# Kernel optimization log

Hardware: AMD Instinct MI355X
Metric: run time of the kernel (lower is better)

## Reference

```python
import jax, jax.numpy as jnp
import numpy as np

N_DATA = 500_000
FEAT_DIM = 512
NUM_CLASS = 10_000
BATCH = 8192
MOMENTUM = 0.9


def setup_inputs() -> dict:
    key = jax.random.key(0)
    k1, k2, k3, k4 = jax.random.split(key, 4)
    stdv = 1.0 / np.sqrt(FEAT_DIM / 3)
    # lat_memory initialized as randn * 2*stdv - stdv (matches torch init)
    lat_memory = jax.random.normal(k1, (N_DATA, FEAT_DIM), dtype=jnp.float32) * (2 * stdv) - stdv
    batch_samples = jax.random.normal(k2, (BATCH, FEAT_DIM), dtype=jnp.float32)
    targets = jax.random.randint(k3, (BATCH,), 0, NUM_CLASS)
    # unique dataset indices (each training sample has one memory slot)
    idx = jax.random.permutation(k4, N_DATA)[:BATCH]
    class_sums = jnp.zeros((NUM_CLASS, FEAT_DIM), dtype=jnp.float32)
    return {
        "batch_samples": batch_samples,
        "lat_memory": lat_memory,
        "class_sums": class_sums,
        "targets": targets,
        "idx": idx,
    }


def reference(batch_samples, lat_memory, class_sums, targets, idx):
    # gather rows, momentum blend, L2 normalize
    blended = lat_memory[idx] * (1.0 - MOMENTUM) + batch_samples * MOMENTUM  # [B, D]
    norm = jnp.sqrt(jnp.sum(blended * blended, axis=1, keepdims=True))
    updated = blended / norm  # [B, D]
    # scatter normalized rows back into the memory bank
    new_lat_memory = lat_memory.at[idx].set(updated)
    # per-class segment sum (replaces python loop over unique labels)
    new_class_sums = class_sums + jax.ops.segment_sum(updated, targets, num_segments=NUM_CLASS)
    return new_lat_memory, new_class_sums
```

## Files before the change

kernel.cpp:

```cpp
#include <hip/hip_runtime.h>

#define N_DATA    500000
#define FEAT_DIM  512
#define NUM_CLASS 10000
#define BATCH     8192
#define MOMENTUM  0.9f

__global__ __launch_bounds__(256) void copy_f4_kernel(const float4* __restrict__ src,
                                                      float4* __restrict__ dst,
                                                      long long n4) {
    long long i = (long long)blockIdx.x * blockDim.x + threadIdx.x;
    long long stride = (long long)gridDim.x * blockDim.x;
    for (; i < n4; i += stride) {
        dst[i] = src[i];
    }
}

__global__ __launch_bounds__(128) void update_kernel(const float4* __restrict__ batch,
                                                     const float4* __restrict__ lat,
                                                     const int*    __restrict__ targets,
                                                     const int*    __restrict__ idx,
                                                     float4*       __restrict__ out_lat,
                                                     float*        __restrict__ out_cls)
{
    const int row = blockIdx.x;
    const int t   = threadIdx.x;

    const int src_row = idx[row];
    const int cls     = targets[row];

    const float4 b = batch[(long long)row * 128 + t];
    const float4 m = lat[(long long)src_row * 128 + t];

    float4 v;
    v.x = m.x * (1.0f - MOMENTUM) + b.x * MOMENTUM;
    v.y = m.y * (1.0f - MOMENTUM) + b.y * MOMENTUM;
    v.z = m.z * (1.0f - MOMENTUM) + b.z * MOMENTUM;
    v.w = m.w * (1.0f - MOMENTUM) + b.w * MOMENTUM;

    float ss = v.x * v.x + v.y * v.y + v.z * v.z + v.w * v.w;

    #pragma unroll
    for (int off = 32; off > 0; off >>= 1) {
        ss += __shfl_down(ss, off, 64);
    }

    __shared__ float partial[2];
    if ((t & 63) == 0) partial[t >> 6] = ss;
    __syncthreads();
    const float total = partial[0] + partial[1];
    const float inv = 1.0f / sqrtf(total);

    v.x *= inv; v.y *= inv; v.z *= inv; v.w *= inv;

    out_lat[(long long)src_row * 128 + t] = v;

    float* cp = out_cls + (long long)cls * FEAT_DIM + t * 4;
    atomicAdd(cp + 0, v.x);
    atomicAdd(cp + 1, v.y);
    atomicAdd(cp + 2, v.z);
    atomicAdd(cp + 3, v.w);
}

extern "C" void kernel_launch(void* const* d_in, const int* in_sizes, int n_in,
                              void* d_out, int out_size, void* d_ws, size_t ws_size,
                              hipStream_t stream) {
    const float* batch    = (const float*)d_in[0];
    const float* lat      = (const float*)d_in[1];
    const float* cls_sums = (const float*)d_in[2];
    const int*   targets  = (const int*)d_in[3];
    const int*   idx      = (const int*)d_in[4];

    float* out_lat = (float*)d_out;
    float* out_cls = out_lat + (long long)N_DATA * FEAT_DIM;

    {
        long long n4 = (long long)N_DATA * FEAT_DIM / 4;
        int blocks = 8192;
        copy_f4_kernel<<<blocks, 256, 0, stream>>>((const float4*)lat, (float4*)out_lat, n4);
    }

    {
        long long n4 = (long long)NUM_CLASS * FEAT_DIM / 4;
        int blocks = 2560;
        copy_f4_kernel<<<blocks, 256, 0, stream>>>((const float4*)cls_sums, (float4*)out_cls, n4);
    }

    update_kernel<<<BATCH, 128, 0, stream>>>((const float4*)batch, (const float4*)lat,
                                             targets, idx,
                                             (float4*)out_lat, out_cls);
}
```

Measured before the change: 1.749 ms.

## Fuse memory-bank copy with row update using a scattered-index bitmap

A prep kernel builds a bitmap of the scattered row indices in workspace and copies class sums. A single fused kernel then gives 1/8 of its blocks to the normalize/update work (one wavefront per row, two float4 per lane, a xor shuffle reduction with no shared memory). The remaining blocks copy the memory bank while skipping rows in the bitmap. This removes the redundant write of overwritten rows and the separate copy→update serialization, at the cost of a bitmap lookup per float4 and depending on a large enough workspace.

```diff
diff --git a/kernel.cpp b/kernel.cpp
--- a/kernel.cpp
+++ b/kernel.cpp
@@ -6,14 +6,109 @@
 #define BATCH     8192
 #define MOMENTUM  0.9f
 
+#define BITMAP_WORDS 15625
+#define FUSED_GRID   2048
+#define UPD_BLOCKS   (FUSED_GRID / 8)
+#define CPY_BLOCKS   (FUSED_GRID - UPD_BLOCKS)
+#define ROWS_PER_UPD (BATCH / UPD_BLOCKS)
+
+__global__ __launch_bounds__(256) void prep_kernel(const float4* __restrict__ cls_src,
+                                                   float4*       __restrict__ cls_dst,
+                                                   const int*    __restrict__ idx,
+                                                   unsigned int* __restrict__ bitmap) {
+    const int t = threadIdx.x;
+    if (blockIdx.x == 0) {
+        for (int i = t; i < BITMAP_WORDS; i += 256) bitmap[i] = 0u;
+        __syncthreads();
+        for (int i = t; i < BATCH; i += 256) {
+            const int r = idx[i];
+            atomicOr(&bitmap[r >> 5], 1u << (r & 31));
+        }
+    } else {
+        const long long n4     = (long long)NUM_CLASS * (FEAT_DIM / 4);
+        const long long stride = (long long)(gridDim.x - 1) * 256;
+        long long i = (long long)(blockIdx.x - 1) * 256 + t;
+        for (; i < n4; i += stride) cls_dst[i] = cls_src[i];
+    }
+}
+
+__global__ __launch_bounds__(256) void fused_kernel(const float4* __restrict__ batch,
+                                                    const float4* __restrict__ lat,
+                                                    const int*    __restrict__ targets,
+                                                    const int*    __restrict__ idx,
+                                                    const unsigned int* __restrict__ bitmap,
+                                                    float4*       __restrict__ out_lat,
+                                                    float*        __restrict__ out_cls)
+{
+    const int t = threadIdx.x;
+    const int b = blockIdx.x;
+
+    if ((b & 7) == 0) {
+        const int upd = b >> 3;
+        const int w   = t >> 6;
+        const int l   = t & 63;
+        #pragma unroll
+        for (int pass = 0; pass < ROWS_PER_UPD / 4; ++pass) {
+            const int row = upd * ROWS_PER_UPD + pass * 4 + w;
+            const int src = idx[row];
+            const int cls = targets[row];
+            const long long bb = (long long)row * 128 + l;
+            const long long mb = (long long)src * 128 + l;
+
+            const float4 b0 = batch[bb], b1 = batch[bb + 64];
+            const float4 m0 = lat[mb],   m1 = lat[mb + 64];
+
+            float4 v0, v1;
+            v0.x = m0.x * (1.0f - MOMENTUM) + b0.x * MOMENTUM;
+            v0.y = m0.y * (1.0f - MOMENTUM) + b0.y * MOMENTUM;
+            v0.z = m0.z * (1.0f - MOMENTUM) + b0.z * MOMENTUM;
+            v0.w = m0.w * (1.0f - MOMENTUM) + b0.w * MOMENTUM;
+            v1.x = m1.x * (1.0f - MOMENTUM) + b1.x * MOMENTUM;
+            v1.y = m1.y * (1.0f - MOMENTUM) + b1.y * MOMENTUM;
+            v1.z = m1.z * (1.0f - MOMENTUM) + b1.z * MOMENTUM;
+            v1.w = m1.w * (1.0f - MOMENTUM) + b1.w * MOMENTUM;
+
+            float ss = v0.x * v0.x + v0.y * v0.y + v0.z * v0.z + v0.w * v0.w
+                     + v1.x * v1.x + v1.y * v1.y + v1.z * v1.z + v1.w * v1.w;
+            #pragma unroll
+            for (int off = 32; off > 0; off >>= 1) ss += __shfl_xor(ss, off, 64);
+            const float inv = 1.0f / sqrtf(ss);
+
+            v0.x *= inv; v0.y *= inv; v0.z *= inv; v0.w *= inv;
+            v1.x *= inv; v1.y *= inv; v1.z *= inv; v1.w *= inv;
+
+            out_lat[mb]      = v0;
+            out_lat[mb + 64] = v1;
+
+            float* cp = out_cls + (long long)cls * FEAT_DIM + 4 * l;
+            atomicAdd(cp + 0, v0.x);
+            atomicAdd(cp + 1, v0.y);
+            atomicAdd(cp + 2, v0.z);
+            atomicAdd(cp + 3, v0.w);
+            atomicAdd(cp + 256 + 0, v1.x);
+            atomicAdd(cp + 256 + 1, v1.y);
+            atomicAdd(cp + 256 + 2, v1.z);
+            atomicAdd(cp + 256 + 3, v1.w);
+        }
+    } else {
+        const int cid = b - (b >> 3) - 1;
+        const long long n4     = (long long)N_DATA * 128;
+        const long long stride = (long long)CPY_BLOCKS * 256;
+        long long i = (long long)cid * 256 + t;
+        for (; i < n4; i += stride) {
+            const int row = (int)(i >> 7);
+            if ((bitmap[row >> 5] >> (row & 31)) & 1u) continue;
+            out_lat[i] = lat[i];
+        }
+    }
+}
+
 __global__ __launch_bounds__(256) void copy_f4_kernel(const float4* __restrict__ src,
                                                       float4* __restrict__ dst,
                                                       long long n4) {
     long long i = (long long)blockIdx.x * blockDim.x + threadIdx.x;
     long long stride = (long long)gridDim.x * blockDim.x;
-    for (; i < n4; i += stride) {
-        dst[i] = src[i];
-    }
+    for (; i < n4; i += stride) dst[i] = src[i];
 }
 
 __global__ __launch_bounds__(128) void update_kernel(const float4* __restrict__ batch,
@@ -25,25 +120,21 @@
 {
     const int row = blockIdx.x;
     const int t   = threadIdx.x;
-
     const int src_row = idx[row];
     const int cls     = targets[row];
 
-    const float4 b = batch[(long long)row * 128 + t];
-    const float4 m = lat[(long long)src_row * 128 + t];
+    const float4 bv = batch[(long long)row * 128 + t];
+    const float4 m  = lat[(long long)src_row * 128 + t];
 
     float4 v;
-    v.x = m.x * (1.0f - MOMENTUM) + b.x * MOMENTUM;
-    v.y = m.y * (1.0f - MOMENTUM) + b.y * MOMENTUM;
-    v.z = m.z * (1.0f - MOMENTUM) + b.z * MOMENTUM;
-    v.w = m.w * (1.0f - MOMENTUM) + b.w * MOMENTUM;
+    v.x = m.x * (1.0f - MOMENTUM) + bv.x * MOMENTUM;
+    v.y = m.y * (1.0f - MOMENTUM) + bv.y * MOMENTUM;
+    v.z = m.z * (1.0f - MOMENTUM) + bv.z * MOMENTUM;
+    v.w = m.w * (1.0f - MOMENTUM) + bv.w * MOMENTUM;
 
     float ss = v.x * v.x + v.y * v.y + v.z * v.z + v.w * v.w;
-
     #pragma unroll
-    for (int off = 32; off > 0; off >>= 1) {
-        ss += __shfl_down(ss, off, 64);
-    }
+    for (int off = 32; off > 0; off >>= 1) ss += __shfl_down(ss, off, 64);
 
     __shared__ float partial[2];
     if ((t & 63) == 0) partial[t >> 6] = ss;
@@ -52,7 +143,6 @@
     const float inv = 1.0f / sqrtf(total);
 
     v.x *= inv; v.y *= inv; v.z *= inv; v.w *= inv;
-
     out_lat[(long long)src_row * 128 + t] = v;
 
     float* cp = out_cls + (long long)cls * FEAT_DIM + t * 4;
@@ -74,19 +164,26 @@
     float* out_lat = (float*)d_out;
     float* out_cls = out_lat + (long long)N_DATA * FEAT_DIM;
 
-    {
-        long long n4 = (long long)N_DATA * FEAT_DIM / 4;
-        int blocks = 8192;
-        copy_f4_kernel<<<blocks, 256, 0, stream>>>((const float4*)lat, (float4*)out_lat, n4);
+    if (ws_size >= (size_t)(BITMAP_WORDS * sizeof(unsigned int))) {
+        unsigned int* bitmap = (unsigned int*)d_ws;
+
+        prep_kernel<<<2561, 256, 0, stream>>>((const float4*)cls_sums, (float4*)out_cls,
+                                              idx, bitmap);
+
+        fused_kernel<<<FUSED_GRID, 256, 0, stream>>>((const float4*)batch, (const float4*)lat,
+                                                     targets, idx, bitmap,
+                                                     (float4*)out_lat, out_cls);
+    } else {
+        {
+            long long n4 = (long long)N_DATA * FEAT_DIM / 4;
+            copy_f4_kernel<<<8192, 256, 0, stream>>>((const float4*)lat, (float4*)out_lat, n4);
+        }
+        {
+            long long n4 = (long long)NUM_CLASS * FEAT_DIM / 4;
+            copy_f4_kernel<<<2560, 256, 0, stream>>>((const float4*)cls_sums, (float4*)out_cls, n4);
+        }
+        update_kernel<<<BATCH, 128, 0, stream>>>((const float4*)batch, (const float4*)lat,
+                                                 targets, idx,
+                                                 (float4*)out_lat, out_cls);
     }
-
-    {
-        long long n4 = (long long)NUM_CLASS * FEAT_DIM / 4;
-        int blocks = 2560;
-        copy_f4_kernel<<<blocks, 256, 0, stream>>>((const float4*)cls_sums, (float4*)out_cls, n4);
-    }
-
-    update_kernel<<<BATCH, 128, 0, stream>>>((const float4*)batch, (const float4*)lat,
-                                             targets, idx,
-                                             (float4*)out_lat, out_cls);
 }
```

New measurement: 1.683 ms. 3.8% less time.
